# Kernel tuning notes

Hardware: AMD Instinct MI355X
Metric: run time of the kernel (lower is better)

The kernel has to match this reference:

```python
import jax, jax.numpy as jnp
import numpy as np

N_NODES = 50000
N_EDGES = 500000
DIM = 128
N_REL = 51
N_LAYERS = 4
B, K = 1024, 32
EPS = 1e-6


def setup_inputs() -> dict:
    key = jax.random.key(0)
    ks = jax.random.split(key, 10)
    x0 = jax.random.normal(ks[0], (N_NODES, DIM), jnp.float32)
    edge_index = jax.random.randint(ks[1], (2, N_EDGES), 0, N_NODES, dtype=jnp.int32)
    edge_type = jax.random.randint(ks[2], (N_EDGES,), 0, N_REL, dtype=jnp.int32)
    edge_weight = jnp.ones((N_EDGES,), jnp.float32)
    rel_w = jax.random.normal(ks[3], (N_LAYERS, N_REL, DIM), jnp.float32) * 0.1
    lin_w = jax.random.normal(ks[4], (N_LAYERS, 13 * DIM, DIM), jnp.float32) * (1.0 / np.sqrt(13 * DIM))
    lin_b = jnp.zeros((N_LAYERS, DIM), jnp.float32)
    ln_g = jnp.ones((N_LAYERS, DIM), jnp.float32)
    ln_b = jnp.zeros((N_LAYERS, DIM), jnp.float32)
    query_w = jax.random.normal(ks[5], (N_REL, DIM), jnp.float32) * 0.1
    src = jax.random.randint(ks[6], (B, K), 0, N_NODES, dtype=jnp.int32)
    rel = jax.random.randint(ks[7], (B, K), 0, N_REL, dtype=jnp.int32)
    dst = jax.random.randint(ks[8], (B, K), 0, N_NODES, dtype=jnp.int32)
    return dict(x0=x0, edge_index=edge_index, edge_type=edge_type, edge_weight=edge_weight,
                rel_w=rel_w, lin_w=lin_w, lin_b=lin_b, ln_g=ln_g, ln_b=ln_b,
                query_w=query_w, src=src, rel=rel, dst=dst)


def _rgcn_forward(x0, edge_weight, rel_w, lin_w, lin_b, ln_g, ln_b, query_w,
                  edge_index, edge_type, src, rel, dst):
    s, d = edge_index[0], edge_index[1]
    # in-degree (each node also gets an implicit boundary self-message)
    deg = jax.ops.segment_sum(jnp.ones((N_EDGES,), x0.dtype), d, num_segments=N_NODES)
    degree_out = deg[:, None] + 1.0  # [N,1]
    scale = jnp.log(degree_out)
    scale = scale / scale.mean()
    # PNA degree scalers: identity, amplification, attenuation  [N,3]
    scales = jnp.concatenate([jnp.ones_like(scale), scale, 1.0 / jnp.clip(scale, 1e-2)], axis=-1)

    x = x0
    for l in range(N_LAYERS):
        # distmult message per edge: [E, D]
        msg = x[s] * rel_w[l][edge_type] * edge_weight[:, None]
        # aggregate with boundary (x0) as self-loop message
        sum_m = jax.ops.segment_sum(msg, d, num_segments=N_NODES) + x0
        sum_sq = jax.ops.segment_sum(msg * msg, d, num_segments=N_NODES) + x0 * x0
        mx = jnp.maximum(jax.ops.segment_max(msg, d, num_segments=N_NODES), x0)
        mn = jnp.minimum(jax.ops.segment_min(msg, d, num_segments=N_NODES), x0)
        mean = sum_m / degree_out
        sq_mean = sum_sq / degree_out
        std = jnp.sqrt(jnp.clip(sq_mean - mean * mean, EPS, None))
        feats = jnp.stack([mean, mx, mn, std], axis=-2)        # [N,4,D]
        out = (feats[:, None, :, :] * scales[:, :, None, None]).reshape(N_NODES, 12 * DIM)
        out = jnp.concatenate([out, x], axis=-1) @ lin_w[l] + lin_b[l]  # [N,D]
        # layer norm
        mu = out.mean(-1, keepdims=True)
        var = out.var(-1, keepdims=True)
        out = (out - mu) / jnp.sqrt(var + 1e-5) * ln_g[l] + ln_b[l]
        out = jax.nn.relu(out)
        x = out + x  # short cut (same shapes)

    # distmult scoring over (src, rel, dst) triples: [B, K]
    return (x[src] * query_w[rel] * x[dst]).sum(-1)


def reference(x0, edge_index, edge_type, edge_weight, rel_w, lin_w, lin_b,
              ln_g, ln_b, query_w, src, rel, dst):
    return _rgcn_forward(x0, edge_weight, rel_w, lin_w, lin_b, ln_g, ln_b, query_w,
                         edge_index, edge_type, src, rel, dst)
```

## Files before the change

### kernel.cpp

```cpp
#include <hip/hip_runtime.h>
#include <math.h>

#define NNODES 50000
#define NEDGES 500000
#define DIM 128
#define NREL 51
#define NLAYERS 4
#define NTRIPLES (1024*32)
#define KDIM 1664
#define TILE_US 8192
#define NBLK 196

typedef float f2 __attribute__((ext_vector_type(2)));
typedef float f32x4 __attribute__((ext_vector_type(4)));
typedef short bf16x8 __attribute__((ext_vector_type(8)));

static __device__ __forceinline__ ushort bf16_rne(float v) {
  unsigned u = __float_as_uint(v);
  unsigned r = (u + 0x7fffu + ((u >> 16) & 1u)) >> 16;
  return (ushort)r;
}
static __device__ __forceinline__ float bf16_f(ushort h) {
  return __uint_as_float(((unsigned)h) << 16);
}
static __device__ __forceinline__ f2 unpack_bf2(uint u) {
  f2 r;
  r.x = __uint_as_float(u << 16);
  r.y = __uint_as_float(u & 0xffff0000u);
  return r;
}
static __device__ __forceinline__ f2 fmax2(f2 a, f2 b) { f2 r; r.x = fmaxf(a.x,b.x); r.y = fmaxf(a.y,b.y); return r; }
static __device__ __forceinline__ f2 fmin2(f2 a, f2 b) { f2 r; r.x = fminf(a.x,b.x); r.y = fminf(a.y,b.y); return r; }

static __device__ __forceinline__ void gload_lds16(const void* g, void* l) {
  __builtin_amdgcn_global_load_lds(
      (const __attribute__((address_space(1))) unsigned int*)g,
      (__attribute__((address_space(3))) unsigned int*)l,
      16, 0, 0);
}


__global__ void deg_hist_k(const int* __restrict__ ei, int* __restrict__ deg) {
  int e = blockIdx.x * blockDim.x + threadIdx.x;
  if (e < NEDGES) atomicAdd(&deg[ei[NEDGES + e]], 1);
}

__global__ void logsum_k(const int* __restrict__ deg, float* __restrict__ acc) {
  int i = blockIdx.x * blockDim.x + threadIdx.x;
  float v = (i < NNODES) ? logf((float)(deg[i] + 1)) : 0.0f;
  #pragma unroll
  for (int m = 32; m >= 1; m >>= 1) v += __shfl_xor(v, m, 64);
  __shared__ float ws[4];
  int lane = threadIdx.x & 63, w = threadIdx.x >> 6;
  if (lane == 0) ws[w] = v;
  __syncthreads();
  if (threadIdx.x == 0) atomicAdd(acc, ws[0] + ws[1] + ws[2] + ws[3]);
}


__global__ __launch_bounds__(256) void blocksum_k(const int* __restrict__ deg,
                                                  int* __restrict__ bsum) {
  int idx = blockIdx.x * 256 + threadIdx.x;
  int v = (idx < NNODES) ? deg[idx] : 0;
  #pragma unroll
  for (int m = 32; m >= 1; m >>= 1) v += __shfl_xor(v, m, 64);
  __shared__ int ws[4];
  int lane = threadIdx.x & 63, w = threadIdx.x >> 6;
  if (lane == 0) ws[w] = v;
  __syncthreads();
  if (threadIdx.x == 0) bsum[blockIdx.x] = ws[0] + ws[1] + ws[2] + ws[3];
}

__global__ __launch_bounds__(256) void bscan_k(const int* __restrict__ bsum,
                                               int* __restrict__ bofs) {
  int t = threadIdx.x;
  int v = (t < NBLK) ? bsum[t] : 0;
  int lane = t & 63, w = t >> 6;
  int sc = v;
  #pragma unroll
  for (int off = 1; off < 64; off <<= 1) {
    int u = __shfl_up(sc, off, 64);
    if (lane >= off) sc += u;
  }
  __shared__ int ws[4];
  if (lane == 63) ws[w] = sc;
  __syncthreads();
  int wo = 0;
  for (int i = 0; i < w; ++i) wo += ws[i];
  if (t < NBLK) bofs[t] = wo + sc - v;
}

__global__ __launch_bounds__(256) void csr_offsets_k(const int* __restrict__ deg,
                                                     const int* __restrict__ bofs,
                                                     int* __restrict__ row_start,
                                                     int* __restrict__ cursor) {
  int t = threadIdx.x;
  int idx = blockIdx.x * 256 + t;
  int v = (idx < NNODES) ? deg[idx] : 0;
  int lane = t & 63, w = t >> 6;
  int sc = v;
  #pragma unroll
  for (int off = 1; off < 64; off <<= 1) {
    int u = __shfl_up(sc, off, 64);
    if (lane >= off) sc += u;
  }
  __shared__ int ws[4];
  if (lane == 63) ws[w] = sc;
  __syncthreads();
  int wo = 0;
  for (int i = 0; i < w; ++i) wo += ws[i];
  int excl = bofs[blockIdx.x] + wo + sc - v;
  if (idx < NNODES) {
    row_start[idx] = excl;
    cursor[idx] = excl;
    if (idx == NNODES - 1) row_start[NNODES] = excl + v;
  }
}

__global__ void scales_k(const int* __restrict__ deg, const float* __restrict__ logsum,
                         float* __restrict__ scales) {
  int i = blockIdx.x * blockDim.x + threadIdx.x;
  if (i >= NNODES) return;
  float mean = *logsum / (float)NNODES;
  float sc = logf((float)(deg[i] + 1)) / mean;
  scales[i*3 + 0] = 1.0f;
  scales[i*3 + 1] = sc;
  scales[i*3 + 2] = 1.0f / fmaxf(sc, 0.01f);
}

__global__ void scatter_k(const int* __restrict__ ei, const int* __restrict__ etype,
                          const float* __restrict__ ew, int* __restrict__ cursor,
                          int* __restrict__ s_srt, int* __restrict__ t_srt,
                          float* __restrict__ w_srt) {
  int e = blockIdx.x * blockDim.x + threadIdx.x;
  if (e >= NEDGES) return;
  int d = ei[NEDGES + e];
  int pos = atomicAdd(&cursor[d], 1);
  s_srt[pos] = ei[e];
  t_srt[pos] = etype[e];
  w_srt[pos] = ew[e];
}


__global__ void wsplit_k(const float* __restrict__ W, ushort* __restrict__ wt) {
  int id = blockIdx.x * blockDim.x + threadIdx.x;
  if (id >= NLAYERS * KDIM * DIM) return;
  int col = id & 127;
  int k = (id >> 7) % KDIM;
  int l = id / (KDIM * DIM);
  float v = W[(size_t)l * KDIM * DIM + (size_t)k * DIM + col];
  ushort h = bf16_rne(v);
  ushort lo = bf16_rne(v - bf16_f(h));
  int c = k >> 5, kk = k & 31;
  int tidx = (c < 48) ? ((c & 15) * 3 + (c >> 4)) : c;
  size_t base = (size_t)((size_t)l * 52 + tidx) * TILE_US;
  int slot = (kk >> 3) ^ ((col >> 1) & 3);
  int off = col * 32 + (slot << 3) + (kk & 7);
  wt[base + off] = h;
  wt[base + 4096 + off] = lo;
}


__global__ void xsplit_k(const float* __restrict__ x, ushort* __restrict__ xh,
                         ushort* __restrict__ xl) {
  int id = blockIdx.x * blockDim.x + threadIdx.x;
  if (id >= NNODES * 64) return;
  f2 v = *(const f2*)(x + (size_t)id * 2);
  ushort h0 = bf16_rne(v.x), h1 = bf16_rne(v.y);
  ushort l0 = bf16_rne(v.x - bf16_f(h0)), l1 = bf16_rne(v.y - bf16_f(h1));
  ((uint*)xh)[id] = (uint)h0 | ((uint)h1 << 16);
  ((uint*)xl)[id] = (uint)l0 | ((uint)l1 << 16);
}


__global__ __launch_bounds__(256) void aggregate_k(
    const ushort* __restrict__ xh, const float* __restrict__ x0,
    const float* __restrict__ relw, const int* __restrict__ row_start,
    const int* __restrict__ s_srt, const int* __restrict__ t_srt,
    const float* __restrict__ w_srt,
    ushort* __restrict__ sh)
{
  int wid = blockIdx.x * 4 + (threadIdx.x >> 6);
  if (wid >= NNODES) return;
  int lane = threadIdx.x & 63;
  int j0 = lane * 2;
  int beg = row_start[wid], end = row_start[wid + 1];
  int deg = end - beg;
  f2 sum = {0.f, 0.f}, sq = {0.f, 0.f};
  f2 mx = {-INFINITY, -INFINITY}, mn = {INFINITY, INFINITY};

  int eidx = beg + lane;
  bool va = eidx < end;
  int   sv = va ? s_srt[eidx] : 0;
  int   tv = va ? t_srt[eidx] : 0;
  float wv = va ? w_srt[eidx] : 0.0f;

  int n = (deg < 64) ? deg : 64;
  int e = 0;
  for (; e + 4 <= n; e += 4) {
    int s0 = __shfl(sv, e, 64),     s1 = __shfl(sv, e + 1, 64);
    int s2 = __shfl(sv, e + 2, 64), s3 = __shfl(sv, e + 3, 64);
    int t0 = __shfl(tv, e, 64),     t1 = __shfl(tv, e + 1, 64);
    int t2 = __shfl(tv, e + 2, 64), t3 = __shfl(tv, e + 3, 64);
    float w0 = __shfl(wv, e, 64),     w1 = __shfl(wv, e + 1, 64);
    float w2 = __shfl(wv, e + 2, 64), w3 = __shfl(wv, e + 3, 64);
    f2 xa = unpack_bf2(*(const uint*)(xh + (size_t)s0 * DIM + j0));
    f2 xb = unpack_bf2(*(const uint*)(xh + (size_t)s1 * DIM + j0));
    f2 xc = unpack_bf2(*(const uint*)(xh + (size_t)s2 * DIM + j0));
    f2 xd = unpack_bf2(*(const uint*)(xh + (size_t)s3 * DIM + j0));
    f2 ra = *(const f2*)(relw + (size_t)t0 * DIM + j0);
    f2 rb = *(const f2*)(relw + (size_t)t1 * DIM + j0);
    f2 rc = *(const f2*)(relw + (size_t)t2 * DIM + j0);
    f2 rd = *(const f2*)(relw + (size_t)t3 * DIM + j0);
    f2 m0 = xa * ra * w0;
    f2 m1 = xb * rb * w1;
    f2 m2 = xc * rc * w2;
    f2 m3 = xd * rd * w3;
    sum += m0 + m1 + m2 + m3;
    sq += m0*m0 + m1*m1 + m2*m2 + m3*m3;
    mx = fmax2(fmax2(fmax2(mx, m0), fmax2(m1, m2)), m3);
    mn = fmin2(fmin2(fmin2(mn, m0), fmin2(m1, m2)), m3);
  }
  for (; e < n; ++e) {
    int s = __shfl(sv, e, 64);
    int ty = __shfl(tv, e, 64);
    float w = __shfl(wv, e, 64);
    f2 xs = unpack_bf2(*(const uint*)(xh + (size_t)s * DIM + j0));
    f2 rv = *(const f2*)(relw + (size_t)ty * DIM + j0);
    f2 m = xs * rv * w;
    sum += m; sq += m * m;
    mx = fmax2(mx, m); mn = fmin2(mn, m);
  }
  for (int ee = beg + 64; ee < end; ++ee) {
    int s = s_srt[ee]; int ty = t_srt[ee]; float w = w_srt[ee];
    f2 xs = unpack_bf2(*(const uint*)(xh + (size_t)s * DIM + j0));
    f2 rv = *(const f2*)(relw + (size_t)ty * DIM + j0);
    f2 m = xs * rv * w;
    sum += m; sq += m * m;
    mx = fmax2(mx, m); mn = fmin2(mn, m);
  }

  f2 x0v = *(const f2*)(x0 + (size_t)wid * DIM + j0);
  sum += x0v; sq += x0v * x0v;
  mx = fmax2(mx, x0v); mn = fmin2(mn, x0v);
  float dq = (float)(deg + 1);
  f2 mean = sum / dq;
  f2 sqm = sq / dq;
  f2 var = sqm - mean * mean;
  f2 sd; sd.x = sqrtf(fmaxf(var.x, 1e-6f)); sd.y = sqrtf(fmaxf(var.y, 1e-6f));
  f2 feats[4] = {mean, mx, mn, sd};
  size_t base = (size_t)wid * 512 + j0;
  #pragma unroll
  for (int f = 0; f < 4; ++f) {
    f2 v = feats[f];
    ushort h0 = bf16_rne(v.x), h1 = bf16_rne(v.y);
    *(uint*)(sh + base + f * 128) = (uint)h0 | ((uint)h1 << 16);
  }
}


__global__ __launch_bounds__(512, 2) void gemm_fused_k(
    const ushort* __restrict__ sh,
    const ushort* __restrict__ xh, const ushort* __restrict__ xl,
    const float* __restrict__ scales, const ushort* __restrict__ wtl,
    const float* __restrict__ bias, const float* __restrict__ gam,
    const float* __restrict__ bet, float* __restrict__ x,
    ushort* __restrict__ xho, ushort* __restrict__ xlo)
{
  __shared__ ushort As[2 * 2048];
  __shared__ ushort Bs[3 * TILE_US];
  int t = threadIdx.x;
  int w = t >> 6, lane = t & 63;
  int lr = lane & 15, lk = lane >> 4;
  int rg = w >> 2, cg = w & 3;
  int row0 = blockIdx.x * 64;

  int th = t & 255;
  int sr = th >> 2, sq = th & 3;
  int an = row0 + sr; if (an >= NNODES) an = NNODES - 1;
  int aoff = sr * 32 + ((sq ^ ((sr >> 1) & 3)) << 3);

  f32x4 p0_00, p0_01, p0_10, p0_11;
  f32x4 p1_00, p1_01, p1_10, p1_11;
  f32x4 p2_00, p2_01, p2_10, p2_11;
  p0_00 = p0_01 = p0_10 = p0_11 = (f32x4){0.f,0.f,0.f,0.f};
  p1_00 = p1_01 = p1_10 = p1_11 = (f32x4){0.f,0.f,0.f,0.f};
  p2_00 = p2_01 = p2_10 = p2_11 = (f32x4){0.f,0.f,0.f,0.f};

  bf16x8 rr;
  auto loadA = [&](int cp) {
    if (t < 256) {
      if (cp < 16) rr = *(const bf16x8*)(sh + (size_t)an * 512 + cp * 32 + sq * 8);
      else         rr = *(const bf16x8*)(xh + (size_t)an * 128 + (cp - 16) * 32 + sq * 8);
    } else if (cp >= 16) {
      rr = *(const bf16x8*)(xl + (size_t)an * 128 + (cp - 16) * 32 + sq * 8);
    }
  };
  auto writeA = [&](int cp) {
    if (t < 256) *(bf16x8*)(As + aoff) = rr;
    else if (cp >= 16) *(bf16x8*)(As + 2048 + aoff) = rr;
  };
  auto issueB = [&](int cp) {
    int tile0 = (cp < 16) ? cp * 3 : cp + 32;
    const char* src = (const char*)(wtl + (size_t)tile0 * TILE_US);
    char* d = (char*)Bs;
    gload_lds16(src + t * 16, d + t * 16);
    gload_lds16(src + (512 + t) * 16, d + (512 + t) * 16);
    if (cp < 16) {
      gload_lds16(src + (1024 + t) * 16, d + (1024 + t) * 16);
      gload_lds16(src + (1536 + t) * 16, d + (1536 + t) * 16);
      gload_lds16(src + (2048 + t) * 16, d + (2048 + t) * 16);
      gload_lds16(src + (2560 + t) * 16, d + (2560 + t) * 16);
    }
  };

  const int ar = rg * 32 + lr;
  const int aswz = ar * 32 + ((lk ^ ((ar >> 1) & 3)) << 3);
  const int bcol = cg * 32 + lr;
  const int bswz = bcol * 32 + ((lk ^ ((bcol >> 1) & 3)) << 3);

#define LOADB(Btile)                                                               \
    const ushort* Bb = (Btile) + bswz;                                             \
    bf16x8 bh0 = *(const bf16x8*)(Bb);                                             \
    bf16x8 bl0 = *(const bf16x8*)(Bb + 4096);                                      \
    bf16x8 bh1 = *(const bf16x8*)(Bb + 512);                                       \
    bf16x8 bl1 = *(const bf16x8*)(Bb + 4096 + 512);

#define MFMA_S2(pa, pb, pc, pd, Btile)                                             \
  {                                                                                \
    LOADB(Btile)                                                                   \
    pa = __builtin_amdgcn_mfma_f32_16x16x32_bf16(ah0, bh0, pa, 0,0,0);             \
    pa = __builtin_amdgcn_mfma_f32_16x16x32_bf16(ah0, bl0, pa, 0,0,0);             \
    pb = __builtin_amdgcn_mfma_f32_16x16x32_bf16(ah0, bh1, pb, 0,0,0);             \
    pb = __builtin_amdgcn_mfma_f32_16x16x32_bf16(ah0, bl1, pb, 0,0,0);             \
    pc = __builtin_amdgcn_mfma_f32_16x16x32_bf16(ah1, bh0, pc, 0,0,0);             \
    pc = __builtin_amdgcn_mfma_f32_16x16x32_bf16(ah1, bl0, pc, 0,0,0);             \
    pd = __builtin_amdgcn_mfma_f32_16x16x32_bf16(ah1, bh1, pd, 0,0,0);             \
    pd = __builtin_amdgcn_mfma_f32_16x16x32_bf16(ah1, bl1, pd, 0,0,0);             \
  }

#define MFMA_S3(pa, pb, pc, pd, Btile)                                             \
  {                                                                                \
    LOADB(Btile)                                                                   \
    pa = __builtin_amdgcn_mfma_f32_16x16x32_bf16(ah0, bh0, pa, 0,0,0);             \
    pa = __builtin_amdgcn_mfma_f32_16x16x32_bf16(ah0, bl0, pa, 0,0,0);             \
    pa = __builtin_amdgcn_mfma_f32_16x16x32_bf16(al0, bh0, pa, 0,0,0);             \
    pb = __builtin_amdgcn_mfma_f32_16x16x32_bf16(ah0, bh1, pb, 0,0,0);             \
    pb = __builtin_amdgcn_mfma_f32_16x16x32_bf16(ah0, bl1, pb, 0,0,0);             \
    pb = __builtin_amdgcn_mfma_f32_16x16x32_bf16(al0, bh1, pb, 0,0,0);             \
    pc = __builtin_amdgcn_mfma_f32_16x16x32_bf16(ah1, bh0, pc, 0,0,0);             \
    pc = __builtin_amdgcn_mfma_f32_16x16x32_bf16(ah1, bl0, pc, 0,0,0);             \
    pc = __builtin_amdgcn_mfma_f32_16x16x32_bf16(al1, bh0, pc, 0,0,0);             \
    pd = __builtin_amdgcn_mfma_f32_16x16x32_bf16(ah1, bh1, pd, 0,0,0);             \
    pd = __builtin_amdgcn_mfma_f32_16x16x32_bf16(ah1, bl1, pd, 0,0,0);             \
    pd = __builtin_amdgcn_mfma_f32_16x16x32_bf16(al1, bh1, pd, 0,0,0);             \
  }

  loadA(0);
  for (int cp = 0; cp < 20; ++cp) {
    __syncthreads();
    writeA(cp);
    issueB(cp);
    if (cp < 19) loadA(cp + 1);
    __syncthreads();
    const ushort* Ab = As + aswz;
    if (cp < 16) {
      bf16x8 ah0 = *(const bf16x8*)(Ab);
      bf16x8 ah1 = *(const bf16x8*)(Ab + 512);
      MFMA_S2(p0_00, p0_01, p0_10, p0_11, Bs);
      MFMA_S2(p1_00, p1_01, p1_10, p1_11, Bs + TILE_US);
      MFMA_S2(p2_00, p2_01, p2_10, p2_11, Bs + 2 * TILE_US);
    } else {
      bf16x8 ah0 = *(const bf16x8*)(Ab);
      bf16x8 al0 = *(const bf16x8*)(Ab + 2048);
      bf16x8 ah1 = *(const bf16x8*)(Ab + 512);
      bf16x8 al1 = *(const bf16x8*)(Ab + 2048 + 512);
      MFMA_S3(p0_00, p0_01, p0_10, p0_11, Bs);
    }
  }
#undef MFMA_S2
#undef MFMA_S3
#undef LOADB

  __syncthreads();
  float* outT = (float*)Bs;
  float bc0 = bias[cg * 32 + lr];
  float bc1 = bias[cg * 32 + 16 + lr];
  f32x4 q0[2][2] = {{p0_00, p0_01}, {p0_10, p0_11}};
  f32x4 q1[2][2] = {{p1_00, p1_01}, {p1_10, p1_11}};
  f32x4 q2[2][2] = {{p2_00, p2_01}, {p2_10, p2_11}};
  #pragma unroll
  for (int fr = 0; fr < 2; ++fr) {
    int lrbase = rg * 32 + fr * 16 + lk * 4;
    #pragma unroll
    for (int q = 0; q < 4; ++q) {
      int lrow = lrbase + q;
      int r = row0 + lrow;
      int rc = (r < NNODES) ? r : (NNODES - 1);
      float s1 = scales[rc * 3 + 1];
      float s2 = scales[rc * 3 + 2];
      outT[lrow * 132 + cg * 32 + lr] =
          q0[fr][0][q] + s1 * q1[fr][0][q] + s2 * q2[fr][0][q] + bc0;
      outT[lrow * 132 + cg * 32 + 16 + lr] =
          q0[fr][1][q] + s1 * q1[fr][1][q] + s2 * q2[fr][1][q] + bc1;
    }
  }
  __syncthreads();

  int j0 = lane * 2;
  f2 g = *(const f2*)(gam + j0);
  f2 be = *(const f2*)(bet + j0);
  for (int rrow = 0; rrow < 8; ++rrow) {
    int lrow = w * 8 + rrow;
    int r = row0 + lrow;
    f2 v;
    v.x = outT[lrow * 132 + j0];
    v.y = outT[lrow * 132 + j0 + 1];
    float s = v.x + v.y;
    float qq = v.x * v.x + v.y * v.y;
    #pragma unroll
    for (int m = 1; m < 64; m <<= 1) { s += __shfl_xor(s, m, 64); qq += __shfl_xor(qq, m, 64); }
    float mu = s * (1.0f / 128.0f);
    float var = qq * (1.0f / 128.0f) - mu * mu;
    float rstd = rsqrtf(var + 1e-5f);
    f2 o = (v - mu) * rstd * g + be;
    o.x = fmaxf(o.x, 0.f); o.y = fmaxf(o.y, 0.f);
    if (r < NNODES) {
      float* xp = x + (size_t)r * DIM + j0;
      f2 xr = *(const f2*)xp;
      f2 res = o + xr;
      *(f2*)xp = res;
      ushort h0 = bf16_rne(res.x), h1 = bf16_rne(res.y);
      ushort l0 = bf16_rne(res.x - bf16_f(h0)), l1 = bf16_rne(res.y - bf16_f(h1));
      *(uint*)(xho + (size_t)r * DIM + j0) = (uint)h0 | ((uint)h1 << 16);
      *(uint*)(xlo + (size_t)r * DIM + j0) = (uint)l0 | ((uint)l1 << 16);
    }
  }
}


__global__ __launch_bounds__(256) void score_k(
    const float* __restrict__ x, const float* __restrict__ qw,
    const int* __restrict__ src, const int* __restrict__ rel,
    const int* __restrict__ dst, float* __restrict__ out)
{
  int wid = blockIdx.x * 4 + (threadIdx.x >> 6);
  if (wid >= NTRIPLES) return;
  int lane = threadIdx.x & 63;
  int j0 = lane * 2;
  int s = src[wid], r = rel[wid], d = dst[wid];
  f2 xs = *(const f2*)(x  + (size_t)s * DIM + j0);
  f2 q  = *(const f2*)(qw + (size_t)r * DIM + j0);
  f2 xd = *(const f2*)(x  + (size_t)d * DIM + j0);
  float p = xs.x*q.x*xd.x + xs.y*q.y*xd.y;
  #pragma unroll
  for (int m = 32; m >= 1; m >>= 1) p += __shfl_xor(p, m, 64);
  if (lane == 0) out[wid] = p;
}


extern "C" void kernel_launch(void* const* d_in, const int* in_sizes, int n_in,
                              void* d_out, int out_size, void* d_ws, size_t ws_size,
                              hipStream_t stream) {
  const float* x0    = (const float*)d_in[0];
  const int*   ei    = (const int*)d_in[1];
  const int*   etyp  = (const int*)d_in[2];
  const float* ew    = (const float*)d_in[3];
  const float* rel_w = (const float*)d_in[4];
  const float* lin_w = (const float*)d_in[5];
  const float* lin_b = (const float*)d_in[6];
  const float* ln_g  = (const float*)d_in[7];
  const float* lnb   = (const float*)d_in[8];
  const float* qw    = (const float*)d_in[9];
  const int*   srcq  = (const int*)d_in[10];
  const int*   relq  = (const int*)d_in[11];
  const int*   dstq  = (const int*)d_in[12];
  float* out = (float*)d_out;

  char* ws = (char*)d_ws;
  size_t off = 0;
  auto alloc = [&](size_t bytes) -> void* {
    void* p = ws + off; off = (off + bytes + 255) & ~(size_t)255; return p;
  };
  int*    deg       = (int*)alloc((size_t)NNODES * 4);
  int*    row_start = (int*)alloc((size_t)(NNODES + 1) * 4);
  int*    cursor    = (int*)alloc((size_t)NNODES * 4);
  int*    bsum      = (int*)alloc((size_t)(NBLK + 1) * 4);
  int*    bofs      = (int*)alloc((size_t)(NBLK + 1) * 4);
  int*    s_srt     = (int*)alloc((size_t)NEDGES * 4);
  int*    t_srt     = (int*)alloc((size_t)NEDGES * 4);
  float*  w_srt     = (float*)alloc((size_t)NEDGES * 4);
  float*  scales    = (float*)alloc((size_t)NNODES * 3 * 4);
  float*  logsum    = (float*)alloc(256);
  ushort* stats_hi  = (ushort*)alloc((size_t)NNODES * 512 * 2);
  float*  xbuf      = (float*)alloc((size_t)NNODES * DIM * 4);
  ushort* xhi       = (ushort*)alloc((size_t)NNODES * DIM * 2);
  ushort* xlo       = (ushort*)alloc((size_t)NNODES * DIM * 2);
  ushort* wtbuf     = (ushort*)alloc((size_t)NLAYERS * 52 * TILE_US * 2);

  hipMemsetAsync(deg, 0, (size_t)NNODES * 4, stream);
  hipMemsetAsync(logsum, 0, 4, stream);
  deg_hist_k<<<(NEDGES + 255) / 256, 256, 0, stream>>>(ei, deg);
  logsum_k<<<(NNODES + 255) / 256, 256, 0, stream>>>(deg, logsum);
  blocksum_k<<<NBLK, 256, 0, stream>>>(deg, bsum);
  bscan_k<<<1, 256, 0, stream>>>(bsum, bofs);
  csr_offsets_k<<<NBLK, 256, 0, stream>>>(deg, bofs, row_start, cursor);
  scales_k<<<(NNODES + 255) / 256, 256, 0, stream>>>(deg, logsum, scales);
  scatter_k<<<(NEDGES + 255) / 256, 256, 0, stream>>>(ei, etyp, ew, cursor, s_srt, t_srt, w_srt);
  wsplit_k<<<(NLAYERS * KDIM * DIM + 255) / 256, 256, 0, stream>>>(lin_w, wtbuf);
  hipMemcpyAsync(xbuf, x0, (size_t)NNODES * DIM * 4, hipMemcpyDeviceToDevice, stream);
  xsplit_k<<<(NNODES * 64 + 255) / 256, 256, 0, stream>>>(x0, xhi, xlo);

  for (int l = 0; l < NLAYERS; ++l) {
    aggregate_k<<<(NNODES + 3) / 4, 256, 0, stream>>>(
        xhi, x0, rel_w + (size_t)l * NREL * DIM, row_start, s_srt, t_srt, w_srt,
        stats_hi);
    gemm_fused_k<<<(NNODES + 63) / 64, 512, 0, stream>>>(
        stats_hi, xhi, xlo, scales, wtbuf + (size_t)l * 52 * TILE_US,
        lin_b + (size_t)l * DIM, ln_g + (size_t)l * DIM, lnb + (size_t)l * DIM,
        xbuf, xhi, xlo);
  }
  score_k<<<(NTRIPLES + 3) / 4, 256, 0, stream>>>(xbuf, qw, srcq, relq, dstq, out);
}
```

Measured before the change: 550.1 us.

## Double GEMM row tile to 128 rows per block to reuse weight tiles

The fused GEMM+LayerNorm kernel now processes 128 node rows per block instead of 64, with each wave computing 64x32 outputs (24 accumulators of f32x4). Every B weight tile loaded into LDS is reused across twice as many rows, halving weight traffic and block count. The epilogue is split into two passes through the shared staging buffer. The extra accumulator registers may raise register pressure under launch_bounds(512,2), and halving the block count reduces parallelism, with 391 blocks on 256 CUs.

```diff
diff --git a/kernel.cpp b/kernel.cpp
--- a/kernel.cpp
+++ b/kernel.cpp
@@ -267,38 +267,37 @@
     const float* __restrict__ bet, float* __restrict__ x,
     ushort* __restrict__ xho, ushort* __restrict__ xlo)
 {
-  __shared__ ushort As[2 * 2048];
+  __shared__ ushort As[2 * 4096];
   __shared__ ushort Bs[3 * TILE_US];
   int t = threadIdx.x;
   int w = t >> 6, lane = t & 63;
   int lr = lane & 15, lk = lane >> 4;
   int rg = w >> 2, cg = w & 3;
-  int row0 = blockIdx.x * 64;
-
-  int th = t & 255;
-  int sr = th >> 2, sq = th & 3;
+  int row0 = blockIdx.x * 128;
+
+  int sr = t >> 2, sq = t & 3;
   int an = row0 + sr; if (an >= NNODES) an = NNODES - 1;
   int aoff = sr * 32 + ((sq ^ ((sr >> 1) & 3)) << 3);
 
-  f32x4 p0_00, p0_01, p0_10, p0_11;
-  f32x4 p1_00, p1_01, p1_10, p1_11;
-  f32x4 p2_00, p2_01, p2_10, p2_11;
-  p0_00 = p0_01 = p0_10 = p0_11 = (f32x4){0.f,0.f,0.f,0.f};
-  p1_00 = p1_01 = p1_10 = p1_11 = (f32x4){0.f,0.f,0.f,0.f};
-  p2_00 = p2_01 = p2_10 = p2_11 = (f32x4){0.f,0.f,0.f,0.f};
-
-  bf16x8 rr;
+  f32x4 a00,a01,a10,a11,a20,a21,a30,a31;
+  f32x4 b00,b01,b10,b11,b20,b21,b30,b31;
+  f32x4 c00,c01,c10,c11,c20,c21,c30,c31;
+  a00=a01=a10=a11=a20=a21=a30=a31=(f32x4){0.f,0.f,0.f,0.f};
+  b00=b01=b10=b11=b20=b21=b30=b31=(f32x4){0.f,0.f,0.f,0.f};
+  c00=c01=c10=c11=c20=c21=c30=c31=(f32x4){0.f,0.f,0.f,0.f};
+
+  bf16x8 rh, rl;
   auto loadA = [&](int cp) {
-    if (t < 256) {
-      if (cp < 16) rr = *(const bf16x8*)(sh + (size_t)an * 512 + cp * 32 + sq * 8);
-      else         rr = *(const bf16x8*)(xh + (size_t)an * 128 + (cp - 16) * 32 + sq * 8);
-    } else if (cp >= 16) {
-      rr = *(const bf16x8*)(xl + (size_t)an * 128 + (cp - 16) * 32 + sq * 8);
+    if (cp < 16) {
+      rh = *(const bf16x8*)(sh + (size_t)an * 512 + cp * 32 + sq * 8);
+    } else {
+      rh = *(const bf16x8*)(xh + (size_t)an * 128 + (cp - 16) * 32 + sq * 8);
+      rl = *(const bf16x8*)(xl + (size_t)an * 128 + (cp - 16) * 32 + sq * 8);
     }
   };
   auto writeA = [&](int cp) {
-    if (t < 256) *(bf16x8*)(As + aoff) = rr;
-    else if (cp >= 16) *(bf16x8*)(As + 2048 + aoff) = rr;
+    *(bf16x8*)(As + aoff) = rh;
+    if (cp >= 16) *(bf16x8*)(As + 4096 + aoff) = rl;
   };
   auto issueB = [&](int cp) {
     int tile0 = (cp < 16) ? cp * 3 : cp + 32;
@@ -314,46 +313,43 @@
     }
   };
 
-  const int ar = rg * 32 + lr;
+  const int ar = rg * 64 + lr;
   const int aswz = ar * 32 + ((lk ^ ((ar >> 1) & 3)) << 3);
   const int bcol = cg * 32 + lr;
   const int bswz = bcol * 32 + ((lk ^ ((bcol >> 1) & 3)) << 3);
 
-#define LOADB(Btile)                                                               \
-    const ushort* Bb = (Btile) + bswz;                                             \
+#define MFMA(d, va, vb) d = __builtin_amdgcn_mfma_f32_16x16x32_bf16(va, vb, d, 0,0,0)
+#define LOADB(BT)                                                                  \
+    const ushort* Bb = (BT) + bswz;                                                \
     bf16x8 bh0 = *(const bf16x8*)(Bb);                                             \
     bf16x8 bl0 = *(const bf16x8*)(Bb + 4096);                                      \
     bf16x8 bh1 = *(const bf16x8*)(Bb + 512);                                       \
     bf16x8 bl1 = *(const bf16x8*)(Bb + 4096 + 512);
 
-#define MFMA_S2(pa, pb, pc, pd, Btile)                                             \
-  {                                                                                \
-    LOADB(Btile)                                                                   \
-    pa = __builtin_amdgcn_mfma_f32_16x16x32_bf16(ah0, bh0, pa, 0,0,0);             \
-    pa = __builtin_amdgcn_mfma_f32_16x16x32_bf16(ah0, bl0, pa, 0,0,0);             \
-    pb = __builtin_amdgcn_mfma_f32_16x16x32_bf16(ah0, bh1, pb, 0,0,0);             \
-    pb = __builtin_amdgcn_mfma_f32_16x16x32_bf16(ah0, bl1, pb, 0,0,0);             \
-    pc = __builtin_amdgcn_mfma_f32_16x16x32_bf16(ah1, bh0, pc, 0,0,0);             \
-    pc = __builtin_amdgcn_mfma_f32_16x16x32_bf16(ah1, bl0, pc, 0,0,0);             \
-    pd = __builtin_amdgcn_mfma_f32_16x16x32_bf16(ah1, bh1, pd, 0,0,0);             \
-    pd = __builtin_amdgcn_mfma_f32_16x16x32_bf16(ah1, bl1, pd, 0,0,0);             \
-  }
-
-#define MFMA_S3(pa, pb, pc, pd, Btile)                                             \
-  {                                                                                \
-    LOADB(Btile)                                                                   \
-    pa = __builtin_amdgcn_mfma_f32_16x16x32_bf16(ah0, bh0, pa, 0,0,0);             \
-    pa = __builtin_amdgcn_mfma_f32_16x16x32_bf16(ah0, bl0, pa, 0,0,0);             \
-    pa = __builtin_amdgcn_mfma_f32_16x16x32_bf16(al0, bh0, pa, 0,0,0);             \
-    pb = __builtin_amdgcn_mfma_f32_16x16x32_bf16(ah0, bh1, pb, 0,0,0);             \
-    pb = __builtin_amdgcn_mfma_f32_16x16x32_bf16(ah0, bl1, pb, 0,0,0);             \
-    pb = __builtin_amdgcn_mfma_f32_16x16x32_bf16(al0, bh1, pb, 0,0,0);             \
-    pc = __builtin_amdgcn_mfma_f32_16x16x32_bf16(ah1, bh0, pc, 0,0,0);             \
-    pc = __builtin_amdgcn_mfma_f32_16x16x32_bf16(ah1, bl0, pc, 0,0,0);             \
-    pc = __builtin_amdgcn_mfma_f32_16x16x32_bf16(al1, bh0, pc, 0,0,0);             \
-    pd = __builtin_amdgcn_mfma_f32_16x16x32_bf16(ah1, bh1, pd, 0,0,0);             \
-    pd = __builtin_amdgcn_mfma_f32_16x16x32_bf16(ah1, bl1, pd, 0,0,0);             \
-    pd = __builtin_amdgcn_mfma_f32_16x16x32_bf16(al1, bh1, pd, 0,0,0);             \
+#define DO_TILE2(P00,P01,P10,P11,P20,P21,P30,P31, BT)                        \
+  {                                                                          \
+    LOADB(BT)                                                                \
+    MFMA(P00, ah0, bh0); MFMA(P00, ah0, bl0);                                \
+    MFMA(P01, ah0, bh1); MFMA(P01, ah0, bl1);                                \
+    MFMA(P10, ah1, bh0); MFMA(P10, ah1, bl0);                                \
+    MFMA(P11, ah1, bh1); MFMA(P11, ah1, bl1);                                \
+    MFMA(P20, ah2, bh0); MFMA(P20, ah2, bl0);                                \
+    MFMA(P21, ah2, bh1); MFMA(P21, ah2, bl1);                                \
+    MFMA(P30, ah3, bh0); MFMA(P30, ah3, bl0);                                \
+    MFMA(P31, ah3, bh1); MFMA(P31, ah3, bl1);                                \
+  }
+
+#define DO_TILE3(P00,P01,P10,P11,P20,P21,P30,P31, BT)                        \
+  {                                                                          \
+    LOADB(BT)                                                                \
+    MFMA(P00, ah0, bh0); MFMA(P00, ah0, bl0); MFMA(P00, al0, bh0);           \
+    MFMA(P01, ah0, bh1); MFMA(P01, ah0, bl1); MFMA(P01, al0, bh1);           \
+    MFMA(P10, ah1, bh0); MFMA(P10, ah1, bl0); MFMA(P10, al1, bh0);           \
+    MFMA(P11, ah1, bh1); MFMA(P11, ah1, bl1); MFMA(P11, al1, bh1);           \
+    MFMA(P20, ah2, bh0); MFMA(P20, ah2, bl0); MFMA(P20, al2, bh0);           \
+    MFMA(P21, ah2, bh1); MFMA(P21, ah2, bl1); MFMA(P21, al2, bh1);           \
+    MFMA(P30, ah3, bh0); MFMA(P30, ah3, bl0); MFMA(P30, al3, bh0);           \
+    MFMA(P31, ah3, bh1); MFMA(P31, ah3, bl1); MFMA(P31, al3, bh1);           \
   }
 
   loadA(0);
@@ -367,73 +363,84 @@
     if (cp < 16) {
       bf16x8 ah0 = *(const bf16x8*)(Ab);
       bf16x8 ah1 = *(const bf16x8*)(Ab + 512);
-      MFMA_S2(p0_00, p0_01, p0_10, p0_11, Bs);
-      MFMA_S2(p1_00, p1_01, p1_10, p1_11, Bs + TILE_US);
-      MFMA_S2(p2_00, p2_01, p2_10, p2_11, Bs + 2 * TILE_US);
+      bf16x8 ah2 = *(const bf16x8*)(Ab + 1024);
+      bf16x8 ah3 = *(const bf16x8*)(Ab + 1536);
+      DO_TILE2(a00,a01,a10,a11,a20,a21,a30,a31, Bs);
+      DO_TILE2(b00,b01,b10,b11,b20,b21,b30,b31, Bs + TILE_US);
+      DO_TILE2(c00,c01,c10,c11,c20,c21,c30,c31, Bs + 2 * TILE_US);
     } else {
       bf16x8 ah0 = *(const bf16x8*)(Ab);
-      bf16x8 al0 = *(const bf16x8*)(Ab + 2048);
       bf16x8 ah1 = *(const bf16x8*)(Ab + 512);
-      bf16x8 al1 = *(const bf16x8*)(Ab + 2048 + 512);
-      MFMA_S3(p0_00, p0_01, p0_10, p0_11, Bs);
+      bf16x8 ah2 = *(const bf16x8*)(Ab + 1024);
+      bf16x8 ah3 = *(const bf16x8*)(Ab + 1536);
+      bf16x8 al0 = *(const bf16x8*)(Ab + 4096);
+      bf16x8 al1 = *(const bf16x8*)(Ab + 4096 + 512);
+      bf16x8 al2 = *(const bf16x8*)(Ab + 4096 + 1024);
+      bf16x8 al3 = *(const bf16x8*)(Ab + 4096 + 1536);
+      DO_TILE3(a00,a01,a10,a11,a20,a21,a30,a31, Bs);
     }
   }
-#undef MFMA_S2
-#undef MFMA_S3
+#undef DO_TILE2
+#undef DO_TILE3
 #undef LOADB
-
-  __syncthreads();
+#undef MFMA
+
   float* outT = (float*)Bs;
   float bc0 = bias[cg * 32 + lr];
   float bc1 = bias[cg * 32 + 16 + lr];
-  f32x4 q0[2][2] = {{p0_00, p0_01}, {p0_10, p0_11}};
-  f32x4 q1[2][2] = {{p1_00, p1_01}, {p1_10, p1_11}};
-  f32x4 q2[2][2] = {{p2_00, p2_01}, {p2_10, p2_11}};
-  #pragma unroll
-  for (int fr = 0; fr < 2; ++fr) {
-    int lrbase = rg * 32 + fr * 16 + lk * 4;
-    #pragma unroll
-    for (int q = 0; q < 4; ++q) {
-      int lrow = lrbase + q;
-      int r = row0 + lrow;
-      int rc = (r < NNODES) ? r : (NNODES - 1);
-      float s1 = scales[rc * 3 + 1];
-      float s2 = scales[rc * 3 + 2];
-      outT[lrow * 132 + cg * 32 + lr] =
-          q0[fr][0][q] + s1 * q1[fr][0][q] + s2 * q2[fr][0][q] + bc0;
-      outT[lrow * 132 + cg * 32 + 16 + lr] =
-          q0[fr][1][q] + s1 * q1[fr][1][q] + s2 * q2[fr][1][q] + bc1;
-    }
-  }
-  __syncthreads();
-
+  f32x4 qa[4][2] = {{a00,a01},{a10,a11},{a20,a21},{a30,a31}};
+  f32x4 qb[4][2] = {{b00,b01},{b10,b11},{b20,b21},{b30,b31}};
+  f32x4 qc[4][2] = {{c00,c01},{c10,c11},{c20,c21},{c30,c31}};
   int j0 = lane * 2;
   f2 g = *(const f2*)(gam + j0);
   f2 be = *(const f2*)(bet + j0);
-  for (int rrow = 0; rrow < 8; ++rrow) {
-    int lrow = w * 8 + rrow;
-    int r = row0 + lrow;
-    f2 v;
-    v.x = outT[lrow * 132 + j0];
-    v.y = outT[lrow * 132 + j0 + 1];
-    float s = v.x + v.y;
-    float qq = v.x * v.x + v.y * v.y;
-    #pragma unroll
-    for (int m = 1; m < 64; m <<= 1) { s += __shfl_xor(s, m, 64); qq += __shfl_xor(qq, m, 64); }
-    float mu = s * (1.0f / 128.0f);
-    float var = qq * (1.0f / 128.0f) - mu * mu;
-    float rstd = rsqrtf(var + 1e-5f);
-    f2 o = (v - mu) * rstd * g + be;
-    o.x = fmaxf(o.x, 0.f); o.y = fmaxf(o.y, 0.f);
-    if (r < NNODES) {
-      float* xp = x + (size_t)r * DIM + j0;
-      f2 xr = *(const f2*)xp;
-      f2 res = o + xr;
-      *(f2*)xp = res;
-      ushort h0 = bf16_rne(res.x), h1 = bf16_rne(res.y);
-      ushort l0 = bf16_rne(res.x - bf16_f(h0)), l1 = bf16_rne(res.y - bf16_f(h1));
-      *(uint*)(xho + (size_t)r * DIM + j0) = (uint)h0 | ((uint)h1 << 16);
-      *(uint*)(xlo + (size_t)r * DIM + j0) = (uint)l0 | ((uint)l1 << 16);
+
+  #pragma unroll
+  for (int pass = 0; pass < 2; ++pass) {
+    __syncthreads();
+    if (rg == pass) {
+      #pragma unroll
+      for (int fr = 0; fr < 4; ++fr) {
+        int lrow = fr * 16 + lk * 4;
+        #pragma unroll
+        for (int q = 0; q < 4; ++q) {
+          int r = row0 + pass * 64 + lrow + q;
+          int rc = (r < NNODES) ? r : (NNODES - 1);
+          float s1 = scales[rc * 3 + 1];
+          float s2 = scales[rc * 3 + 2];
+          outT[(lrow + q) * 132 + cg * 32 + lr] =
+              qa[fr][0][q] + s1 * qb[fr][0][q] + s2 * qc[fr][0][q] + bc0;
+          outT[(lrow + q) * 132 + cg * 32 + 16 + lr] =
+              qa[fr][1][q] + s1 * qb[fr][1][q] + s2 * qc[fr][1][q] + bc1;
+        }
+      }
+    }
+    __syncthreads();
+    for (int rrow = 0; rrow < 8; ++rrow) {
+      int lrow = w * 8 + rrow;
+      int r = row0 + pass * 64 + lrow;
+      f2 v;
+      v.x = outT[lrow * 132 + j0];
+      v.y = outT[lrow * 132 + j0 + 1];
+      float s = v.x + v.y;
+      float qq = v.x * v.x + v.y * v.y;
+      #pragma unroll
+      for (int m = 1; m < 64; m <<= 1) { s += __shfl_xor(s, m, 64); qq += __shfl_xor(qq, m, 64); }
+      float mu = s * (1.0f / 128.0f);
+      float var = qq * (1.0f / 128.0f) - mu * mu;
+      float rstd = rsqrtf(var + 1e-5f);
+      f2 o = (v - mu) * rstd * g + be;
+      o.x = fmaxf(o.x, 0.f); o.y = fmaxf(o.y, 0.f);
+      if (r < NNODES) {
+        float* xp = x + (size_t)r * DIM + j0;
+        f2 xr = *(const f2*)xp;
+        f2 res = o + xr;
+        *(f2*)xp = res;
+        ushort h0 = bf16_rne(res.x), h1 = bf16_rne(res.y);
+        ushort l0 = bf16_rne(res.x - bf16_f(h0)), l1 = bf16_rne(res.y - bf16_f(h1));
+        *(uint*)(xho + (size_t)r * DIM + j0) = (uint)h0 | ((uint)h1 << 16);
+        *(uint*)(xlo + (size_t)r * DIM + j0) = (uint)l0 | ((uint)l1 << 16);
+      }
     }
   }
 }
@@ -515,7 +522,7 @@
     aggregate_k<<<(NNODES + 3) / 4, 256, 0, stream>>>(
         xhi, x0, rel_w + (size_t)l * NREL * DIM, row_start, s_srt, t_srt, w_srt,
         stats_hi);
-    gemm_fused_k<<<(NNODES + 63) / 64, 512, 0, stream>>>(
+    gemm_fused_k<<<(NNODES + 127) / 128, 512, 0, stream>>>(
         stats_hi, xhi, xlo, scales, wtbuf + (size_t)l * 52 * TILE_US,
         lin_b + (size_t)l * DIM, ln_g + (size_t)l * DIM, lnb + (size_t)l * DIM,
         xbuf, xhi, xlo);
```

Result: slower. 607.4 us (+10.4%).
